# Optimization experiments

Measured on AMD Instinct MI355X. Metric: run time of the kernel, lower is better.

## Reference

```python
import jax, jax.numpy as jnp
import numpy as np

N_ATOMS = 100000
N_BONDS = 200000
MAX_NB = 6
ATOM_FDIM = 133
BOND_FDIM = 147
HIDDEN = 300
DEPTH = 3
N_MOLS = 4000


def setup_inputs() -> dict:
    key = jax.random.key(0)
    ks = jax.random.split(key, 10)
    f_atoms = jax.random.normal(ks[0], (N_ATOMS, ATOM_FDIM), dtype=jnp.float32)
    f_bonds = jax.random.normal(ks[1], (N_BONDS, BOND_FDIM), dtype=jnp.float32)
    a2b = jax.random.randint(ks[2], (N_ATOMS, MAX_NB), 0, N_BONDS, dtype=jnp.int32)
    b2a = jax.random.randint(ks[3], (N_BONDS,), 0, N_ATOMS, dtype=jnp.int32)
    b2revb = jax.random.randint(ks[4], (N_BONDS,), 0, N_BONDS, dtype=jnp.int32)
    mol_ids = jnp.sort(jax.random.randint(ks[5], (N_ATOMS,), 0, N_MOLS, dtype=jnp.int32))
    # learned params (W_i, W_h have bias=False; W_o has bias)
    sc = 0.02
    W_i = jax.random.normal(ks[6], (BOND_FDIM, HIDDEN), dtype=jnp.float32) * sc
    W_h = jax.random.normal(ks[7], (HIDDEN, HIDDEN), dtype=jnp.float32) * sc
    W_o = jax.random.normal(ks[8], (ATOM_FDIM + HIDDEN, HIDDEN), dtype=jnp.float32) * sc
    b_o = jax.random.normal(ks[9], (HIDDEN,), dtype=jnp.float32) * sc
    return {"f_atoms": f_atoms, "f_bonds": f_bonds, "a2b": a2b, "b2a": b2a,
            "b2revb": b2revb, "mol_ids": mol_ids, "W_i": W_i, "W_h": W_h,
            "W_o": W_o, "b_o": b_o}


def reference(f_atoms, f_bonds, a2b, b2a, b2revb, mol_ids, W_i, W_h, W_o, b_o):
    # input = W_i(f_bonds); message = relu(input)
    inp = f_bonds @ W_i                              # [n_bonds, H]
    message = jax.nn.relu(inp)
    for _ in range(DEPTH - 1):
        # gather incoming-bond messages per atom and sum over neighbors
        a_message = message[a2b].sum(axis=1)         # [n_atoms, H]
        # directed-bond update: m_b = sum_in(src atom) - reverse message
        message = a_message[b2a] - message[b2revb]   # [n_bonds, H]
        message = jax.nn.relu(inp + message @ W_h)   # dropout p=0 -> identity
    a_message = message[a2b].sum(axis=1)             # [n_atoms, H]
    a_input = jnp.concatenate([f_atoms, a_message], axis=1)
    atom_hiddens = jax.nn.relu(a_input @ W_o + b_o)  # [n_atoms, H]
    # per-molecule mean aggregation (a_scope loop -> segment ops)
    sums = jax.ops.segment_sum(atom_hiddens, mol_ids, num_segments=N_MOLS)
    counts = jax.ops.segment_sum(jnp.ones((atom_hiddens.shape[0], 1), atom_hiddens.dtype),
                                 mol_ids, num_segments=N_MOLS)
    # empty molecules -> cached zero vector
    return jnp.where(counts > 0, sums / jnp.maximum(counts, 1.0), 0.0)
```

## Files before the change

### kernel.cpp

```cpp
#include <hip/hip_runtime.h>

typedef unsigned short bfraw;
typedef __attribute__((ext_vector_type(8))) short short8v;
typedef __attribute__((ext_vector_type(8))) unsigned short ushort8v;
typedef __attribute__((ext_vector_type(4))) float f32x4;

static __device__ __forceinline__ float bf2f(unsigned short u) {
    union { unsigned int i; float f; } c; c.i = ((unsigned int)u) << 16; return c.f;
}
static __device__ __forceinline__ unsigned short f2bf(float f) {
    union { float f; unsigned int i; } c; c.f = f;
    unsigned int r = c.i + 0x7fffu + ((c.i >> 16) & 1u);
    return (unsigned short)(r >> 16);
}
static __device__ __forceinline__ unsigned short brelu(unsigned short u) {
    return (u & 0x8000u) ? (unsigned short)0 : u;
}
static __device__ __forceinline__ f32x4 mfma16(short8v a, short8v b, f32x4 c) {
    return __builtin_amdgcn_mfma_f32_16x16x32_bf16(a, b, c, 0, 0, 0);
}

__global__ __launch_bounds__(64) void k_pack(const float* __restrict__ W, int Krows, int row_off,
                                             bfraw* __restrict__ out) {
    const int b = blockIdx.x;
    const int ks = b / 20, ct = b - ks * 20;
    const int l = threadIdx.x;
    const int n = ct * 16 + (l & 15);
    const int kb = ks * 32 + (l >> 4) * 8;
    short8v pk;
#pragma unroll
    for (int j = 0; j < 8; ++j) {
        int k = kb + j;
        float v = (k < Krows && n < 300) ? W[(row_off + k) * 300 + n] : 0.f;
        pk[j] = (short)f2bf(v);
    }
    *(short8v*)&out[(b * 64 + l) * 8] = pk;
}


__global__ __launch_bounds__(512, 4) void k_in(const float* __restrict__ fb,
                                               const bfraw* __restrict__ Wp,
                                               bfraw* __restrict__ inp) {
    __shared__ short A[64 * 40 * 8];
    const int row0 = blockIdx.x * 64;
    const int tid = threadIdx.x;
    if (tid < 128) {
        int r = tid >> 1, c = 18 + (tid & 1);
        short8v z = {0, 0, 0, 0, 0, 0, 0, 0};
        *(short8v*)&A[(r * 40 + (c ^ (r & 7))) * 8] = z;
    }
    __syncthreads();
    const float4* fb4 = (const float4*)(fb + (long long)row0 * 147);
#pragma unroll 1
    for (int s = 0; s < 5; ++s) {
        int idx = tid + s * 512;
        if (idx < 2352) {
            float4 v = fb4[idx];
            const float* ve = (const float*)&v;
            int k0 = idx * 4;
#pragma unroll
            for (int e = 0; e < 4; ++e) {
                int k = k0 + e;
                int r = k / 147;
                int c = k - r * 147;
                A[(r * 40 + ((c >> 3) ^ (r & 7))) * 8 + (c & 7)] = (short)f2bf(ve[e]);
            }
        }
    }
    __syncthreads();
    const int w = tid >> 6, l = tid & 63;
    const int wr = w >> 2, wc = w & 3;
    const int lr = l & 15, lk = l >> 4, sw = l & 7;
    f32x4 acc[2][5];
#pragma unroll
    for (int ri = 0; ri < 2; ++ri)
#pragma unroll
        for (int i = 0; i < 5; ++i) acc[ri][i] = (f32x4){0.f, 0.f, 0.f, 0.f};
    const short8v* Ald = (const short8v*)A;
#pragma unroll
    for (int ks = 0; ks < 5; ++ks) {
        short8v bfr[2], wv[5];
#pragma unroll
        for (int ri = 0; ri < 2; ++ri)
            bfr[ri] = Ald[((wr * 2 + ri) * 16 + lr) * 40 + ((ks * 4 + lk) ^ sw)];
#pragma unroll
        for (int i = 0; i < 5; ++i)
            wv[i] = *(const short8v*)&Wp[((ks * 20 + wc * 5 + i) * 64 + l) * 8];
#pragma unroll
        for (int ri = 0; ri < 2; ++ri)
#pragma unroll
            for (int i = 0; i < 5; ++i)
                acc[ri][i] = mfma16(wv[i], bfr[ri], acc[ri][i]);
    }
    __syncthreads();
#pragma unroll
    for (int ri = 0; ri < 2; ++ri)
#pragma unroll
        for (int i = 0; i < 5; ++i) {
            const int r = (wr * 2 + ri) * 16 + lr;
            const int c16 = (wc * 5 + i) * 2 + (lk >> 1);
            ushort4 t;
            t.x = f2bf(acc[ri][i][0]); t.y = f2bf(acc[ri][i][1]);
            t.z = f2bf(acc[ri][i][2]); t.w = f2bf(acc[ri][i][3]);
            *(ushort4*)&A[(r * 40 + (c16 ^ (r & 7))) * 8 + (lk & 1) * 4] = t;
        }
    __syncthreads();
    for (int idx = tid; idx < 64 * 38; idx += 512) {
        int r = idx / 38, c = idx - r * 38;
        short8v t = *(const short8v*)&A[(r * 40 + (c ^ (r & 7))) * 8];
        *(short8v*)&inp[(long long)(row0 + r) * 304 + c * 8] = t;
    }
}

__global__ __launch_bounds__(256) void k_gather(const bfraw* __restrict__ msg,
                                                const int* __restrict__ a2b,
                                                bfraw* __restrict__ amsg) {
    int gid = blockIdx.x * 256 + threadIdx.x;
    if (gid >= 100000 * 19) return;
    int a = gid / 19, c = gid - a * 19;
    const int* nb = a2b + a * 6;
    float s0[8], s1[8];
#pragma unroll
    for (int e = 0; e < 8; ++e) { s0[e] = 0.f; s1[e] = 0.f; }
#pragma unroll
    for (int j = 0; j < 6; ++j) {
        const long long base = (long long)nb[j] * 304;
        const ushort8v v0 = *(const ushort8v*)&msg[base + c * 8];
        const ushort8v v1 = *(const ushort8v*)&msg[base + (c + 19) * 8];
#pragma unroll
        for (int e = 0; e < 8; ++e) {
            s0[e] += bf2f(brelu(v0[e]));
            s1[e] += bf2f(brelu(v1[e]));
        }
    }
    short8v o0, o1;
#pragma unroll
    for (int e = 0; e < 8; ++e) { o0[e] = (short)f2bf(s0[e]); o1[e] = (short)f2bf(s1[e]); }
    *(short8v*)&amsg[(long long)a * 304 + c * 8] = o0;
    *(short8v*)&amsg[(long long)a * 304 + (c + 19) * 8] = o1;
}

__global__ __launch_bounds__(512, 4) void k_bond(const bfraw* __restrict__ amsg,
                                                 const bfraw* __restrict__ msg,
                                                 const bfraw* __restrict__ inp,
                                                 const int* __restrict__ b2a,
                                                 const int* __restrict__ b2revb,
                                                 const bfraw* __restrict__ Wp,
                                                 bfraw* __restrict__ out) {
    __shared__ short A[64 * 40 * 8];
    const int row0 = blockIdx.x * 64;
    const int tid = threadIdx.x;
    if (tid < 128) {
        int r = tid >> 1, c = 38 + (tid & 1);
        short8v z = {0, 0, 0, 0, 0, 0, 0, 0};
        *(short8v*)&A[(r * 40 + (c ^ (r & 7))) * 8] = z;
    }
    int rr[5], cc[5], ia[5], irv[5];
#pragma unroll
    for (int s = 0; s < 5; ++s) {
        int idx = tid + s * 512;
        if (s < 4 || idx < 2432) {
            rr[s] = idx / 38; cc[s] = idx - rr[s] * 38;
            const int b = row0 + rr[s];
            ia[s] = b2a[b];
            irv[s] = b2revb[b];
        }
    }
    ushort8v va[5], vm[5];
#pragma unroll
    for (int s = 0; s < 5; ++s) {
        int idx = tid + s * 512;
        if (s < 4 || idx < 2432) {
            va[s] = *(const ushort8v*)&amsg[(long long)ia[s] * 304 + cc[s] * 8];
            vm[s] = *(const ushort8v*)&msg[(long long)irv[s] * 304 + cc[s] * 8];
        }
    }
#pragma unroll
    for (int s = 0; s < 5; ++s) {
        int idx = tid + s * 512;
        if (s < 4 || idx < 2432) {
            short8v pk;
#pragma unroll
            for (int j = 0; j < 8; ++j)
                pk[j] = (short)f2bf(bf2f(va[s][j]) - bf2f(brelu(vm[s][j])));
            *(short8v*)&A[(rr[s] * 40 + (cc[s] ^ (rr[s] & 7))) * 8] = pk;
        }
    }
    __syncthreads();
    const int w = tid >> 6, l = tid & 63;
    const int wr = w >> 2, wc = w & 3;
    const int lr = l & 15, lk = l >> 4, sw = l & 7;
    f32x4 acc[2][5];
#pragma unroll
    for (int ri = 0; ri < 2; ++ri)
#pragma unroll
        for (int i = 0; i < 5; ++i) acc[ri][i] = (f32x4){0.f, 0.f, 0.f, 0.f};
    const short8v* Ald = (const short8v*)A;
#pragma unroll
    for (int ks = 0; ks < 10; ++ks) {
        short8v bfr[2], wv[5];
#pragma unroll
        for (int ri = 0; ri < 2; ++ri)
            bfr[ri] = Ald[((wr * 2 + ri) * 16 + lr) * 40 + ((ks * 4 + lk) ^ sw)];
#pragma unroll
        for (int i = 0; i < 5; ++i)
            wv[i] = *(const short8v*)&Wp[((ks * 20 + wc * 5 + i) * 64 + l) * 8];
#pragma unroll
        for (int ri = 0; ri < 2; ++ri)
#pragma unroll
            for (int i = 0; i < 5; ++i)
                acc[ri][i] = mfma16(wv[i], bfr[ri], acc[ri][i]);
    }
    __syncthreads();
#pragma unroll
    for (int ri = 0; ri < 2; ++ri)
#pragma unroll
        for (int i = 0; i < 5; ++i) {
            const int r = (wr * 2 + ri) * 16 + lr;
            const int c16 = (wc * 5 + i) * 2 + (lk >> 1);
            ushort4 t;
            t.x = f2bf(acc[ri][i][0]); t.y = f2bf(acc[ri][i][1]);
            t.z = f2bf(acc[ri][i][2]); t.w = f2bf(acc[ri][i][3]);
            *(ushort4*)&A[(r * 40 + (c16 ^ (r & 7))) * 8 + (lk & 1) * 4] = t;
        }
    __syncthreads();
    ushort8v ip[5];
#pragma unroll
    for (int s = 0; s < 5; ++s) {
        int idx = tid + s * 512;
        if (s < 4 || idx < 2432) {
            int r = idx / 38, c = idx - r * 38;
            ip[s] = *(const ushort8v*)&inp[(long long)(row0 + r) * 304 + c * 8];
        }
    }
#pragma unroll
    for (int s = 0; s < 5; ++s) {
        int idx = tid + s * 512;
        if (s < 4 || idx < 2432) {
            int r = idx / 38, c = idx - r * 38;
            short8v t = *(const short8v*)&A[(r * 40 + (c ^ (r & 7))) * 8];
            short8v m;
#pragma unroll
            for (int j = 0; j < 8; ++j)
                m[j] = (short)f2bf(bf2f(ip[s][j]) + bf2f((unsigned short)t[j]));
            *(short8v*)&out[(long long)(row0 + r) * 304 + c * 8] = m;
        }
    }
}

__global__ __launch_bounds__(512, 4) void k_out(const float* __restrict__ fa,
                                                const bfraw* __restrict__ msg,
                                                const int* __restrict__ a2b,
                                                const bfraw* __restrict__ WfP,
                                                const bfraw* __restrict__ WaP,
                                                const float* __restrict__ bo,
                                                bfraw* __restrict__ hid) {
    __shared__ short A[64 * 40 * 8];
    const int row0 = blockIdx.x * 64;
    const int tid = threadIdx.x;
    const int nvalid = (row0 + 64 <= 100000) ? 64 : (100000 - row0);
#pragma unroll 1
    for (int sp = 0; sp < 5; sp += 2) {
        ushort8v v[2][6];
        int ur[2], uc[2], act[2];
#pragma unroll
        for (int u = 0; u < 2; ++u) {
            act[u] = 0;
            int s = sp + u;
            if (s < 5) {
                int idx = tid + s * 512;
                int r = idx / 40, c = idx - r * 40;
                ur[u] = r; uc[u] = c;
                const int row = row0 + r;
                if (c < 38 && row < 100000) {
                    act[u] = 1;
                    const int* nb = a2b + row * 6;
#pragma unroll
                    for (int j = 0; j < 6; ++j)
                        v[u][j] = *(const ushort8v*)&msg[(long long)nb[j] * 304 + c * 8];
                }
            }
        }
#pragma unroll
        for (int u = 0; u < 2; ++u) {
            int s = sp + u;
            if (s >= 5) continue;
            short8v pk;
            if (act[u]) {
                float sm[8];
#pragma unroll
                for (int e = 0; e < 8; ++e) sm[e] = 0.f;
#pragma unroll
                for (int j = 0; j < 6; ++j)
#pragma unroll
                    for (int e = 0; e < 8; ++e) sm[e] += bf2f(brelu(v[u][j][e]));
#pragma unroll
                for (int e = 0; e < 8; ++e) pk[e] = (short)f2bf(sm[e]);
            } else {
#pragma unroll
                for (int e = 0; e < 8; ++e) pk[e] = 0;
            }
            *(short8v*)&A[(ur[u] * 40 + (uc[u] ^ (ur[u] & 7))) * 8] = pk;
        }
    }
    __syncthreads();
    const int w = tid >> 6, l = tid & 63;
    const int wr = w >> 2, wc = w & 3;
    const int lr = l & 15, lk = l >> 4, sw = l & 7;
    f32x4 acc[2][5];
#pragma unroll
    for (int ri = 0; ri < 2; ++ri)
#pragma unroll
        for (int i = 0; i < 5; ++i) acc[ri][i] = (f32x4){0.f, 0.f, 0.f, 0.f};
    const short8v* Ald = (const short8v*)A;
#pragma unroll
    for (int ks = 0; ks < 10; ++ks) {
        short8v bfr[2], wv[5];
#pragma unroll
        for (int ri = 0; ri < 2; ++ri)
            bfr[ri] = Ald[((wr * 2 + ri) * 16 + lr) * 40 + ((ks * 4 + lk) ^ sw)];
#pragma unroll
        for (int i = 0; i < 5; ++i)
            wv[i] = *(const short8v*)&WaP[((ks * 20 + wc * 5 + i) * 64 + l) * 8];
#pragma unroll
        for (int ri = 0; ri < 2; ++ri)
#pragma unroll
            for (int i = 0; i < 5; ++i)
                acc[ri][i] = mfma16(wv[i], bfr[ri], acc[ri][i]);
    }
    __syncthreads();
    if (tid < 256) {
        int r = tid >> 2, c = 16 + (tid & 3);
        short8v z = {0, 0, 0, 0, 0, 0, 0, 0};
        *(short8v*)&A[(r * 40 + (c ^ (r & 7))) * 8] = z;
    }
    __syncthreads();
    {
        const float4* fa4 = (const float4*)(fa + (long long)row0 * 133);
        const int limit4 = (nvalid * 133) >> 2;
#pragma unroll 1
        for (int s = 0; s < 5; ++s) {
            int idx = tid + s * 512;
            if (idx < limit4) {
                float4 v = fa4[idx];
                const float* ve = (const float*)&v;
                int k0 = idx * 4;
#pragma unroll
                for (int e = 0; e < 4; ++e) {
                    int k = k0 + e;
                    int r = k / 133;
                    int c = k - r * 133;
                    A[(r * 40 + ((c >> 3) ^ (r & 7))) * 8 + (c & 7)] = (short)f2bf(ve[e]);
                }
            }
        }
    }
    __syncthreads();
#pragma unroll
    for (int ks = 0; ks < 5; ++ks) {
        short8v bfr[2], wv[5];
#pragma unroll
        for (int ri = 0; ri < 2; ++ri)
            bfr[ri] = Ald[((wr * 2 + ri) * 16 + lr) * 40 + ((ks * 4 + lk) ^ sw)];
#pragma unroll
        for (int i = 0; i < 5; ++i)
            wv[i] = *(const short8v*)&WfP[((ks * 20 + wc * 5 + i) * 64 + l) * 8];
#pragma unroll
        for (int ri = 0; ri < 2; ++ri)
#pragma unroll
            for (int i = 0; i < 5; ++i)
                acc[ri][i] = mfma16(wv[i], bfr[ri], acc[ri][i]);
    }
    __syncthreads();
#pragma unroll
    for (int ri = 0; ri < 2; ++ri)
#pragma unroll
        for (int i = 0; i < 5; ++i) {
            const int r = (wr * 2 + ri) * 16 + lr;
            const int c16 = (wc * 5 + i) * 2 + (lk >> 1);
            ushort4 t;
            t.x = f2bf(acc[ri][i][0]); t.y = f2bf(acc[ri][i][1]);
            t.z = f2bf(acc[ri][i][2]); t.w = f2bf(acc[ri][i][3]);
            *(ushort4*)&A[(r * 40 + (c16 ^ (r & 7))) * 8 + (lk & 1) * 4] = t;
        }
    __syncthreads();
    for (int idx = tid; idx < 64 * 38; idx += 512) {
        int r = idx / 38, c = idx - r * 38;
        const int row = row0 + r;
        if (row >= 100000) continue;
        short8v t = *(const short8v*)&A[(r * 40 + (c ^ (r & 7))) * 8];
        float4 b0 = *(const float4*)&bo[c * 8];
        float4 b1 = (c < 37) ? *(const float4*)&bo[c * 8 + 4]
                             : make_float4(0.f, 0.f, 0.f, 0.f);
        float bias[8] = {b0.x, b0.y, b0.z, b0.w, b1.x, b1.y, b1.z, b1.w};
        short8v m;
#pragma unroll
        for (int j = 0; j < 8; ++j)
            m[j] = (short)f2bf(fmaxf(bf2f((unsigned short)t[j]) + bias[j], 0.f));
        *(short8v*)&hid[(long long)row * 304 + c * 8] = m;
    }
}

__global__ __launch_bounds__(320) void k_mean(const bfraw* __restrict__ hid,
                                              const int* __restrict__ mol,
                                              float* __restrict__ out) {
    __shared__ float red[8][304];
    const int m = blockIdx.x;
    const int natoms = 100000;
    int lo = 0, hi = natoms;
    while (lo < hi) { int mid = (lo + hi) >> 1; if (mol[mid] < m) lo = mid + 1; else hi = mid; }
    const int start = lo;
    lo = start; hi = natoms;
    while (lo < hi) { int mid = (lo + hi) >> 1; if (mol[mid] <= m) lo = mid + 1; else hi = mid; }
    const int end = lo;
    const int tid = threadIdx.x;
    const int p = tid / 38, c = tid - p * 38;
    if (tid < 304) {
        float s[8];
#pragma unroll
        for (int e = 0; e < 8; ++e) s[e] = 0.f;
        for (int a = start + p; a < end; a += 8) {
            const ushort8v v = *(const ushort8v*)&hid[(long long)a * 304 + c * 8];
#pragma unroll
            for (int e = 0; e < 8; ++e) s[e] += bf2f(v[e]);
        }
#pragma unroll
        for (int e = 0; e < 8; ++e) red[p][c * 8 + e] = s[e];
    }
    __syncthreads();
    if (tid < 300) {
        float t = 0.f;
#pragma unroll
        for (int p2 = 0; p2 < 8; ++p2) t += red[p2][tid];
        const int n = end - start;
        out[m * 300 + tid] = (n > 0) ? (t / (float)n) : 0.f;
    }
}

extern "C" void kernel_launch(void* const* d_in, const int* in_sizes, int n_in,
                              void* d_out, int out_size, void* d_ws, size_t ws_size,
                              hipStream_t stream) {
    const float* f_atoms = (const float*)d_in[0];
    const float* f_bonds = (const float*)d_in[1];
    const int* a2b      = (const int*)d_in[2];
    const int* b2a      = (const int*)d_in[3];
    const int* b2revb   = (const int*)d_in[4];
    const int* mol_ids  = (const int*)d_in[5];
    const float* W_i    = (const float*)d_in[6];
    const float* W_h    = (const float*)d_in[7];
    const float* W_o    = (const float*)d_in[8];
    const float* b_o    = (const float*)d_in[9];
    float* out = (float*)d_out;

    char* wsb = (char*)d_ws;
    bfraw* inp  = (bfraw*)(wsb);
    bfraw* M1   = (bfraw*)(wsb + 121600000ll);
    bfraw* M2   = (bfraw*)(wsb + 243200000ll);
    bfraw* amsg = (bfraw*)(wsb + 364800000ll);
    bfraw* WiP   = (bfraw*)(wsb + 425600000ll);
    bfraw* WhP   = (bfraw*)(wsb + 425702400ll);
    bfraw* WoFaP = (bfraw*)(wsb + 425907200ll);
    bfraw* WoAmP = (bfraw*)(wsb + 426009600ll);

    k_pack<<<100, 64, 0, stream>>>(W_i, 147, 0, WiP);
    k_pack<<<200, 64, 0, stream>>>(W_h, 300, 0, WhP);
    k_pack<<<100, 64, 0, stream>>>(W_o, 133, 0, WoFaP);
    k_pack<<<200, 64, 0, stream>>>(W_o, 300, 133, WoAmP);

    const int nb_blocks = 200000 / 64;
    const int na_blocks = (100000 + 63) / 64;
    const int gather_blocks = (100000 * 19 + 255) / 256;

    k_in<<<nb_blocks, 512, 0, stream>>>(f_bonds, WiP, inp);

    k_gather<<<gather_blocks, 256, 0, stream>>>(inp, a2b, amsg);
    k_bond<<<nb_blocks, 512, 0, stream>>>(amsg, inp, inp, b2a, b2revb, WhP, M1);
    k_gather<<<gather_blocks, 256, 0, stream>>>(M1, a2b, amsg);
    k_bond<<<nb_blocks, 512, 0, stream>>>(amsg, M1, inp, b2a, b2revb, WhP, M2);

    bfraw* hid = M1;
    k_out<<<na_blocks, 512, 0, stream>>>(f_atoms, M2, a2b, WoFaP, WoAmP, b_o, hid);
    k_mean<<<4000, 320, 0, stream>>>(hid, mol_ids, out);
}
```

Measured before the change: 603.1 us.

## Make bond kernel wave-independent with per-wave 16-row tiles, no block barriers

```diff
diff --git a/kernel.cpp b/kernel.cpp
--- a/kernel.cpp
+++ b/kernel.cpp
@@ -36,7 +36,6 @@
     }
     *(short8v*)&out[(b * 64 + l) * 8] = pk;
 }
-
 
 __global__ __launch_bounds__(512, 4) void k_in(const float* __restrict__ fb,
                                                const bfraw* __restrict__ Wp,
@@ -147,103 +146,85 @@
                                                  const int* __restrict__ b2revb,
                                                  const bfraw* __restrict__ Wp,
                                                  bfraw* __restrict__ out) {
-    __shared__ short A[64 * 40 * 8];
-    const int row0 = blockIdx.x * 64;
+    __shared__ short A[128 * 40 * 8];
     const int tid = threadIdx.x;
-    if (tid < 128) {
-        int r = tid >> 1, c = 38 + (tid & 1);
+    const int w = tid >> 6, l = tid & 63;
+    const int wrow0 = blockIdx.x * 128 + w * 16;
+    short* Aw = A + w * 16 * 40 * 8;
+    const int lr = l & 15, lk = l >> 4, sw = l & 7;
+    if (l < 32) {
+        int r = l >> 1, c = 38 + (l & 1);
         short8v z = {0, 0, 0, 0, 0, 0, 0, 0};
-        *(short8v*)&A[(r * 40 + (c ^ (r & 7))) * 8] = z;
-    }
-    int rr[5], cc[5], ia[5], irv[5];
-#pragma unroll
-    for (int s = 0; s < 5; ++s) {
-        int idx = tid + s * 512;
-        if (s < 4 || idx < 2432) {
-            rr[s] = idx / 38; cc[s] = idx - rr[s] * 38;
-            const int b = row0 + rr[s];
-            ia[s] = b2a[b];
-            irv[s] = b2revb[b];
-        }
-    }
-    ushort8v va[5], vm[5];
-#pragma unroll
-    for (int s = 0; s < 5; ++s) {
-        int idx = tid + s * 512;
-        if (s < 4 || idx < 2432) {
-            va[s] = *(const ushort8v*)&amsg[(long long)ia[s] * 304 + cc[s] * 8];
-            vm[s] = *(const ushort8v*)&msg[(long long)irv[s] * 304 + cc[s] * 8];
-        }
-    }
-#pragma unroll
-    for (int s = 0; s < 5; ++s) {
-        int idx = tid + s * 512;
-        if (s < 4 || idx < 2432) {
-            short8v pk;
-#pragma unroll
-            for (int j = 0; j < 8; ++j)
-                pk[j] = (short)f2bf(bf2f(va[s][j]) - bf2f(brelu(vm[s][j])));
-            *(short8v*)&A[(rr[s] * 40 + (cc[s] ^ (rr[s] & 7))) * 8] = pk;
-        }
-    }
-    __syncthreads();
-    const int w = tid >> 6, l = tid & 63;
-    const int wr = w >> 2, wc = w & 3;
-    const int lr = l & 15, lk = l >> 4, sw = l & 7;
-    f32x4 acc[2][5];
-#pragma unroll
-    for (int ri = 0; ri < 2; ++ri)
-#pragma unroll
-        for (int i = 0; i < 5; ++i) acc[ri][i] = (f32x4){0.f, 0.f, 0.f, 0.f};
-    const short8v* Ald = (const short8v*)A;
+        *(short8v*)&Aw[(r * 40 + (c ^ (r & 7))) * 8] = z;
+    }
+#pragma unroll
+    for (int g = 0; g < 2; ++g) {
+        int rr[5], cc[5];
+        ushort8v va[5], vm[5];
+#pragma unroll
+        for (int u = 0; u < 5; ++u) {
+            int idx = l + (g * 5 + u) * 64;
+            rr[u] = idx / 38; cc[u] = idx - rr[u] * 38;
+            int b = wrow0 + rr[u];
+            int ok = (idx < 608) && (b < 200000);
+            int ia  = ok ? b2a[b] : 0;
+            int irv = ok ? b2revb[b] : 0;
+            va[u] = *(const ushort8v*)&amsg[(long long)ia * 304 + cc[u] * 8];
+            vm[u] = *(const ushort8v*)&msg[(long long)irv * 304 + cc[u] * 8];
+        }
+#pragma unroll
+        for (int u = 0; u < 5; ++u) {
+            int idx = l + (g * 5 + u) * 64;
+            if (idx < 608) {
+                short8v pk;
+#pragma unroll
+                for (int j = 0; j < 8; ++j)
+                    pk[j] = (short)f2bf(bf2f(va[u][j]) - bf2f(brelu(vm[u][j])));
+                *(short8v*)&Aw[(rr[u] * 40 + (cc[u] ^ (rr[u] & 7))) * 8] = pk;
+            }
+        }
+    }
+    f32x4 acc[20];
+#pragma unroll
+    for (int i = 0; i < 20; ++i) acc[i] = (f32x4){0.f, 0.f, 0.f, 0.f};
+    const short8v* Awl = (const short8v*)Aw;
 #pragma unroll
     for (int ks = 0; ks < 10; ++ks) {
-        short8v bfr[2], wv[5];
-#pragma unroll
-        for (int ri = 0; ri < 2; ++ri)
-            bfr[ri] = Ald[((wr * 2 + ri) * 16 + lr) * 40 + ((ks * 4 + lk) ^ sw)];
-#pragma unroll
-        for (int i = 0; i < 5; ++i)
-            wv[i] = *(const short8v*)&Wp[((ks * 20 + wc * 5 + i) * 64 + l) * 8];
-#pragma unroll
-        for (int ri = 0; ri < 2; ++ri)
+        short8v af = Awl[lr * 40 + ((ks * 4 + lk) ^ sw)];
+#pragma unroll
+        for (int i0 = 0; i0 < 20; i0 += 5) {
+            short8v wv[5];
 #pragma unroll
             for (int i = 0; i < 5; ++i)
-                acc[ri][i] = mfma16(wv[i], bfr[ri], acc[ri][i]);
-    }
-    __syncthreads();
-#pragma unroll
-    for (int ri = 0; ri < 2; ++ri)
-#pragma unroll
-        for (int i = 0; i < 5; ++i) {
-            const int r = (wr * 2 + ri) * 16 + lr;
-            const int c16 = (wc * 5 + i) * 2 + (lk >> 1);
-            ushort4 t;
-            t.x = f2bf(acc[ri][i][0]); t.y = f2bf(acc[ri][i][1]);
-            t.z = f2bf(acc[ri][i][2]); t.w = f2bf(acc[ri][i][3]);
-            *(ushort4*)&A[(r * 40 + (c16 ^ (r & 7))) * 8 + (lk & 1) * 4] = t;
-        }
-    __syncthreads();
-    ushort8v ip[5];
-#pragma unroll
-    for (int s = 0; s < 5; ++s) {
-        int idx = tid + s * 512;
-        if (s < 4 || idx < 2432) {
+                wv[i] = *(const short8v*)&Wp[((ks * 20 + i0 + i) * 64 + l) * 8];
+#pragma unroll
+            for (int i = 0; i < 5; ++i)
+                acc[i0 + i] = mfma16(wv[i], af, acc[i0 + i]);
+        }
+    }
+#pragma unroll
+    for (int i = 0; i < 20; ++i) {
+        const int c16 = i * 2 + (lk >> 1);
+        ushort4 t;
+        t.x = f2bf(acc[i][0]); t.y = f2bf(acc[i][1]);
+        t.z = f2bf(acc[i][2]); t.w = f2bf(acc[i][3]);
+        *(ushort4*)&Aw[(lr * 40 + (c16 ^ (lr & 7))) * 8 + (lk & 1) * 4] = t;
+    }
+#pragma unroll
+    for (int u = 0; u < 10; ++u) {
+        int idx = l + u * 64;
+        if (idx < 608) {
             int r = idx / 38, c = idx - r * 38;
-            ip[s] = *(const ushort8v*)&inp[(long long)(row0 + r) * 304 + c * 8];
-        }
-    }
-#pragma unroll
-    for (int s = 0; s < 5; ++s) {
-        int idx = tid + s * 512;
-        if (s < 4 || idx < 2432) {
-            int r = idx / 38, c = idx - r * 38;
-            short8v t = *(const short8v*)&A[(r * 40 + (c ^ (r & 7))) * 8];
-            short8v m;
-#pragma unroll
-            for (int j = 0; j < 8; ++j)
-                m[j] = (short)f2bf(bf2f(ip[s][j]) + bf2f((unsigned short)t[j]));
-            *(short8v*)&out[(long long)(row0 + r) * 304 + c * 8] = m;
+            const long long row = wrow0 + r;
+            if (row < 200000) {
+                short8v t = *(const short8v*)&Aw[(r * 40 + (c ^ (r & 7))) * 8];
+                const ushort8v ip = *(const ushort8v*)&inp[row * 304 + c * 8];
+                short8v m;
+#pragma unroll
+                for (int j = 0; j < 8; ++j)
+                    m[j] = (short)f2bf(bf2f(ip[j]) + bf2f((unsigned short)t[j]));
+                *(short8v*)&out[row * 304 + c * 8] = m;
+            }
         }
     }
 }
@@ -468,15 +449,16 @@
     k_pack<<<200, 64, 0, stream>>>(W_o, 300, 133, WoAmP);
 
     const int nb_blocks = 200000 / 64;
+    const int nb2_blocks = (200000 + 127) / 128;
     const int na_blocks = (100000 + 63) / 64;
     const int gather_blocks = (100000 * 19 + 255) / 256;
 
     k_in<<<nb_blocks, 512, 0, stream>>>(f_bonds, WiP, inp);
 
     k_gather<<<gather_blocks, 256, 0, stream>>>(inp, a2b, amsg);
-    k_bond<<<nb_blocks, 512, 0, stream>>>(amsg, inp, inp, b2a, b2revb, WhP, M1);
+    k_bond<<<nb2_blocks, 512, 0, stream>>>(amsg, inp, inp, b2a, b2revb, WhP, M1);
     k_gather<<<gather_blocks, 256, 0, stream>>>(M1, a2b, amsg);
-    k_bond<<<nb_blocks, 512, 0, stream>>>(amsg, M1, inp, b2a, b2revb, WhP, M2);
+    k_bond<<<nb2_blocks, 512, 0, stream>>>(amsg, M1, inp, b2a, b2revb, WhP, M2);
 
     bfraw* hid = M1;
     k_out<<<na_blocks, 512, 0, stream>>>(f_atoms, M2, a2b, WoFaP, WoAmP, b_o, hid);
```

After: 947.4 us. +57.1%, slower.
